# Kernel optimization log

Hardware: AMD Instinct MI355X
Metric: run time of the kernel (lower is better)

Reference implementation:

```python
import jax, jax.numpy as jnp
import numpy as np

B, S, E, D = 8, 2048, 1024, 512

def setup_inputs() -> dict:
    key = jax.random.key(0)
    ks = jax.random.split(key, 7)
    scale = 1.0 / np.sqrt(E)
    return {
        "X": jax.random.normal(ks[0], (B, S, E), dtype=jnp.float32),
        "lam": jnp.float32(0.8),
        "W_q": jax.random.uniform(ks[1], (E, 2 * D), jnp.float32, -scale, scale),
        "b_q": jax.random.uniform(ks[2], (2 * D,), jnp.float32, -scale, scale),
        "W_k": jax.random.uniform(ks[3], (E, 2 * D), jnp.float32, -scale, scale),
        "b_k": jax.random.uniform(ks[4], (2 * D,), jnp.float32, -scale, scale),
        "W_v": jax.random.uniform(ks[5], (E, D), jnp.float32, -scale, scale),
        "b_v": jax.random.uniform(ks[6], (D,), jnp.float32, -scale, scale),
    }

def reference(X, lam, W_q, b_q, W_k, b_k, W_v, b_v):
    # Projections
    Q = X @ W_q + b_q          # [B, S, 2D]
    K = X @ W_k + b_k          # [B, S, 2D]
    V = X @ W_v + b_v          # [B, S, D]
    Q1, Q2 = Q[..., :D], Q[..., D:]
    K1, K2 = K[..., :D], K[..., D:]
    s = 1.0 / np.sqrt(D)
    A1 = jnp.einsum('bqd,bkd->bqk', Q1, K1) * s  # [B, S, S]
    A2 = jnp.einsum('bqd,bkd->bqk', Q2, K2) * s
    P = jax.nn.softmax(A1, axis=-1) - lam * jax.nn.softmax(A2, axis=-1)
    return jnp.einsum('bqk,bkd->bqd', P, V)      # [B, S, D]
```

## Files before the change

kernel.cpp:

```cpp
#include <hip/hip_runtime.h>


typedef unsigned short u16;
typedef short    bf16x8 __attribute__((ext_vector_type(8)));
typedef unsigned short u16x8 __attribute__((ext_vector_type(8)));
typedef unsigned short u16x4 __attribute__((ext_vector_type(4)));
typedef float    f32x4  __attribute__((ext_vector_type(4)));

typedef __attribute__((address_space(3))) unsigned int       lds_uint;
typedef __attribute__((address_space(1))) const unsigned int gl_uint;

__device__ __forceinline__ void glds16(const void* g, void* l) {
  __builtin_amdgcn_global_load_lds((gl_uint*)g, (lds_uint*)l, 16, 0, 0);
}

__device__ __forceinline__ u16 to_bf16(float f) {
  unsigned u = __float_as_uint(f);
  return (u16)((u + 0x7FFFu + ((u >> 16) & 1u)) >> 16);
}
__device__ __forceinline__ float b2f(u16 h) {
  return __uint_as_float(((unsigned)h) << 16);
}


__global__ void cvt_x(const float4* __restrict__ in, u16x4* __restrict__ out, int n4) {
  int i = blockIdx.x * 256 + threadIdx.x;
  if (i >= n4) return;
  float4 v = in[i];
  u16x4 o;
  o[0] = to_bf16(v.x); o[1] = to_bf16(v.y); o[2] = to_bf16(v.z); o[3] = to_bf16(v.w);
  out[i] = o;
}

__global__ void transpose_cvt(const float* __restrict__ in, u16* __restrict__ out,
                              int R, int C) {
  __shared__ float t[64][65];
  int c0 = blockIdx.x * 64, r0 = blockIdx.y * 64;
  int tx = threadIdx.x, ty = threadIdx.y;
  #pragma unroll
  for (int i = 0; i < 64; i += 4)
    t[ty + i][tx] = in[(long)(r0 + ty + i) * C + c0 + tx];
  __syncthreads();
  #pragma unroll
  for (int i = 0; i < 64; i += 4)
    out[(long)(c0 + ty + i) * R + r0 + tx] = to_bf16(t[tx][ty + i]);
}

__global__ void concat2(const float* __restrict__ a, const float* __restrict__ b,
                        float* __restrict__ o, int n) {
  int i = blockIdx.x * 256 + threadIdx.x;
  if (i < n) o[i] = a[i];
  else if (i < 2 * n) o[i] = b[i - n];
}

__device__ __forceinline__ void swizzle_tiles(int& tm, int& tn) {
  int nx = gridDim.x;
  int lin = blockIdx.y * nx + blockIdx.x;
  int span = nx * 4;
  int group = lin / span;
  int ing = lin % span;
  tm = group * 4 + (ing & 3);
  tn = ing >> 2;
}

__global__ __launch_bounds__(256, 4) void gemm_nt(
    const u16* __restrict__ A, int lda,
    const u16* __restrict__ B, int ldb,
    u16* __restrict__ C1, u16* __restrict__ C2, int splitN, int ldc,
    int Kd, float scale,
    const float* __restrict__ bias, int biasMode)
{
  __shared__ u16 SM[2][8192];
  u16* As = SM[0];
  u16* Bs = SM[1];

  int tid = threadIdx.x;
  int wave = tid >> 6, lane = tid & 63;
  int quad = lane >> 4, ln = lane & 15;
  int wm = wave >> 1, wn = wave & 1;
  int tm, tn;
  swizzle_tiles(tm, tn);
  int c8 = lane >> 3, ml = lane & 7;

  const f32x4 fz = {0.f, 0.f, 0.f, 0.f};
  f32x4 acc[4][4];
  #pragma unroll
  for (int i = 0; i < 4; i++)
    #pragma unroll
    for (int j = 0; j < 4; j++) acc[i][j] = fz;

  const u16* Abase = A + (long)(tm * 128 + ml) * lda + c8 * 8;
  const u16* Bbase = B + (long)(tn * 128 + ml) * ldb + c8 * 8;

  for (int kt = 0; kt < Kd; kt += 64) {
    __syncthreads();
    #pragma unroll
    for (int i = 0; i < 4; i++) {
      int mg = wave * 4 + i;
      glds16(Abase + (long)mg * 8 * lda + kt, &As[mg * 512]);
      glds16(Bbase + (long)mg * 8 * ldb + kt, &Bs[mg * 512]);
    }
    __syncthreads();
    #pragma unroll
    for (int ks = 0; ks < 2; ks++) {
      bf16x8 af[4], bfr[4];
      int c = ks * 4 + quad;
      #pragma unroll
      for (int mt = 0; mt < 4; mt++) {
        int m = wm * 64 + mt * 16 + ln;
        af[mt] = *(const bf16x8*)&As[((m >> 3) * 64 + c * 8 + (m & 7)) * 8];
      }
      #pragma unroll
      for (int nt = 0; nt < 4; nt++) {
        int n = wn * 64 + nt * 16 + ln;
        bfr[nt] = *(const bf16x8*)&Bs[((n >> 3) * 64 + c * 8 + (n & 7)) * 8];
      }
      #pragma unroll
      for (int mt = 0; mt < 4; mt++)
        #pragma unroll
        for (int nt = 0; nt < 4; nt++)
          acc[mt][nt] = __builtin_amdgcn_mfma_f32_16x16x32_bf16(af[mt], bfr[nt], acc[mt][nt], 0, 0, 0);
    }
  }

  int rowBase = tm * 128 + wm * 64;
  int colBase = tn * 128 + wn * 64;
  u16* Cw = C1; int outCol = colBase;
  if (colBase >= splitN) { Cw = C2; outCol = colBase - splitN; }
  u16* eb = &SM[0][0] + wave * 4096;

  __syncthreads();
  #pragma unroll
  for (int mt = 0; mt < 4; mt++) {
    #pragma unroll
    for (int nt = 0; nt < 4; nt++) {
      int colL = nt * 16 + ln;
      float bcol = (biasMode == 1) ? bias[colBase + colL] : 0.f;
      #pragma unroll
      for (int r = 0; r < 4; r++) {
        int rowL = mt * 16 + quad * 4 + r;
        float brow = (biasMode == 2) ? bias[rowBase + rowL] : 0.f;
        float v = acc[mt][nt][r] * scale + bcol + brow;
        eb[rowL * 64 + (((colL >> 3) ^ (rowL & 7)) << 3) + (colL & 7)] = to_bf16(v);
      }
    }
  }
  {
    int row = lane;
    long gr = (long)(rowBase + row) * ldc + outCol;
    #pragma unroll
    for (int c = 0; c < 8; c++) {
      u16x8 ch = *(const u16x8*)&eb[row * 64 + ((c ^ (row & 7)) << 3)];
      *(u16x8*)&Cw[gr + c * 8] = ch;
    }
  }
}

__device__ __forceinline__ void gemm256_core(
    const u16* __restrict__ A, int lda,
    const u16* __restrict__ B, int ldb,
    int NT, int tm, int tn, u16* SMp, f32x4 (&acc)[8][4])
{
  int tid = threadIdx.x;
  int wave = tid >> 6, lane = tid & 63;
  int quad = lane >> 4, ln = lane & 15;
  int wm = wave >> 2, wn = wave & 3;
  int c8 = lane >> 3, ml = lane & 7;

  const f32x4 fz = {0.f, 0.f, 0.f, 0.f};
  #pragma unroll
  for (int i = 0; i < 8; i++)
    #pragma unroll
    for (int j = 0; j < 4; j++) acc[i][j] = fz;

  const u16* Ab = A + (long)(tm * 256 + ml) * lda + c8 * 8;
  const u16* Bb = B + (long)(tn * 256 + ml) * ldb + c8 * 8;

  #pragma unroll
  for (int h = 0; h < 2; h++) {
    int hg = h * 16 + wave * 2;
    glds16(Ab + (long)(hg * 8) * lda,       SMp + hg * 512);
    glds16(Ab + (long)(hg * 8 + 8) * lda,   SMp + (hg + 1) * 512);
  }
  #pragma unroll
  for (int h = 0; h < 2; h++) {
    int hg = h * 16 + wave * 2;
    glds16(Bb + (long)(hg * 8) * ldb,       SMp + 32768 + hg * 512);
    glds16(Bb + (long)(hg * 8 + 8) * ldb,   SMp + 32768 + (hg + 1) * 512);
  }
  {
    int kt1 = (NT > 1) ? 64 : 0;
    #pragma unroll
    for (int h = 0; h < 2; h++) {
      int hg = h * 16 + wave * 2;
      glds16(Bb + (long)(hg * 8) * ldb + kt1,     SMp + 49152 + hg * 512);
      glds16(Bb + (long)(hg * 8 + 8) * ldb + kt1, SMp + 49152 + (hg + 1) * 512);
    }
  }
  asm volatile("s_waitcnt vmcnt(4)" ::: "memory");
  __builtin_amdgcn_s_barrier();
  __builtin_amdgcn_sched_barrier(0);

  int bcur = 0;
  for (int t = 0; t < NT; t++) {
    const int p = t & 1;
    const u16* Ar = SMp + p * 16384;
    const u16* Br = SMp + 32768 + bcur * 16384;

    {
      int ktA = ((t + 1 < NT) ? (t + 1) : (NT - 1)) << 6;
      u16* dA = SMp + ((t + 1) & 1) * 16384;
      #pragma unroll
      for (int h = 0; h < 2; h++) {
        int hg = h * 16 + wave * 2;
        glds16(Ab + (long)(hg * 8) * lda + ktA,     dA + hg * 512);
        glds16(Ab + (long)(hg * 8 + 8) * lda + ktA, dA + (hg + 1) * 512);
      }
      int ktB = ((t + 2 < NT) ? (t + 2) : (NT - 1)) << 6;
      int bst = bcur + 2; if (bst >= 3) bst -= 3;
      u16* dB = SMp + 32768 + bst * 16384;
      #pragma unroll
      for (int h = 0; h < 2; h++) {
        int hg = h * 16 + wave * 2;
        glds16(Bb + (long)(hg * 8) * ldb + ktB,     dB + hg * 512);
        glds16(Bb + (long)(hg * 8 + 8) * ldb + ktB, dB + (hg + 1) * 512);
      }
    }
    __builtin_amdgcn_sched_barrier(0);

    bf16x8 bfr[2][4];
    #pragma unroll
    for (int nt = 0; nt < 4; nt++) {
      int n = wn * 64 + nt * 16 + ln;
      #pragma unroll
      for (int ks = 0; ks < 2; ks++)
        bfr[ks][nt] = *(const bf16x8*)(Br + ((n >> 3) * 64 + (ks * 4 + quad) * 8 + (n & 7)) * 8);
    }
    #pragma unroll
    for (int g = 0; g < 4; g++) {
      bf16x8 af[2][2];
      #pragma unroll
      for (int dm = 0; dm < 2; dm++) {
        int m = wm * 128 + (g * 2 + dm) * 16 + ln;
        #pragma unroll
        for (int ks = 0; ks < 2; ks++)
          af[dm][ks] = *(const bf16x8*)(Ar + ((m >> 3) * 64 + (ks * 4 + quad) * 8 + (m & 7)) * 8);
      }
      #pragma unroll
      for (int ks = 0; ks < 2; ks++)
        #pragma unroll
        for (int dm = 0; dm < 2; dm++)
          #pragma unroll
          for (int nt = 0; nt < 4; nt++)
            acc[g * 2 + dm][nt] = __builtin_amdgcn_mfma_f32_16x16x32_bf16(
                af[dm][ks], bfr[ks][nt], acc[g * 2 + dm][nt], 0, 0, 0);
    }

    asm volatile("s_waitcnt vmcnt(4)" ::: "memory");
    __builtin_amdgcn_s_barrier();
    __builtin_amdgcn_sched_barrier(0);
    bcur = (bcur == 2) ? 0 : bcur + 1;
  }
}

__global__ __launch_bounds__(512, 2) void gemm_nt256(
    const u16* __restrict__ A, int lda,
    const u16* __restrict__ B, int ldb,
    u16* __restrict__ C1, u16* __restrict__ C2, int splitN, int ldc,
    int Kd, float scale,
    const float* __restrict__ bias, int biasMode)
{
  __shared__ u16 SM[5][16384];
  int tm, tn;
  swizzle_tiles(tm, tn);
  f32x4 acc[8][4];
  gemm256_core(A, lda, B, ldb, Kd >> 6, tm, tn, &SM[0][0], acc);

  int tid = threadIdx.x;
  int wave = tid >> 6, lane = tid & 63;
  int quad = lane >> 4, ln = lane & 15;
  int wm = wave >> 2, wn = wave & 3;

  int rowBase = tm * 256 + wm * 128;
  int colBase = tn * 256 + wn * 64;
  u16* Cw = C1; int outCol = colBase;
  if (colBase >= splitN) { Cw = C2; outCol = colBase - splitN; }
  u16* eb = &SM[0][0] + wave * 8192;

  asm volatile("s_waitcnt vmcnt(0)" ::: "memory");
  __builtin_amdgcn_s_barrier();
  __builtin_amdgcn_sched_barrier(0);

  #pragma unroll
  for (int mt = 0; mt < 8; mt++) {
    #pragma unroll
    for (int nt = 0; nt < 4; nt++) {
      int colL = nt * 16 + ln;
      float bcol = (biasMode == 1) ? bias[colBase + colL] : 0.f;
      #pragma unroll
      for (int r = 0; r < 4; r++) {
        int rowL = mt * 16 + quad * 4 + r;
        float brow = (biasMode == 2) ? bias[rowBase + rowL] : 0.f;
        float v = acc[mt][nt][r] * scale + bcol + brow;
        eb[rowL * 64 + (((colL >> 3) ^ (rowL & 7)) << 3) + (colL & 7)] = to_bf16(v);
      }
    }
  }
  #pragma unroll
  for (int rr = 0; rr < 2; rr++) {
    int row = rr * 64 + lane;
    long gr = (long)(rowBase + row) * ldc + outCol;
    #pragma unroll
    for (int c = 0; c < 8; c++) {
      u16x8 ch = *(const u16x8*)&eb[row * 64 + ((c ^ (row & 7)) << 3)];
      *(u16x8*)&Cw[gr + c * 8] = ch;
    }
  }
}

__global__ __launch_bounds__(512, 2) void gemm_s256(
    const u16* __restrict__ Q, const u16* __restrict__ K,
    u16* __restrict__ E1, u16* __restrict__ E2,
    float* __restrict__ statsP, float scale)
{
  __shared__ u16 SM[5][16384];
  int bz = blockIdx.z >> 1, half = blockIdx.z & 1;
  const u16* A = Q + (long)bz * 2097152 + half * 512;
  const u16* B = K + (long)bz * 2097152 + half * 512;
  u16* Ed = (half ? E2 : E1) + (long)bz * 4194304;
  statsP += (long)blockIdx.z * 65536;

  int tm, tn;
  swizzle_tiles(tm, tn);
  f32x4 acc[8][4];
  gemm256_core(A, 1024, B, 1024, 8 , tm, tn, &SM[0][0], acc);

  int tid = threadIdx.x;
  int wave = tid >> 6, lane = tid & 63;
  int quad = lane >> 4, ln = lane & 15;
  int wm = wave >> 2, wn = wave & 3;

  int rowBase = tm * 256 + wm * 128;
  int colBase = tn * 256 + wn * 64;
  int kb = tn * 4 + wn;
  u16* eb = &SM[0][0] + wave * 8192;

  asm volatile("s_waitcnt vmcnt(0)" ::: "memory");
  __builtin_amdgcn_s_barrier();
  __builtin_amdgcn_sched_barrier(0);

  #pragma unroll
  for (int mt = 0; mt < 8; mt++) {
    #pragma unroll
    for (int nt = 0; nt < 4; nt++) {
      int colL = nt * 16 + ln;
      #pragma unroll
      for (int r = 0; r < 4; r++) {
        int rowL = mt * 16 + quad * 4 + r;
        eb[rowL * 64 + (((colL >> 3) ^ (rowL & 7)) << 3) + (colL & 7)] =
            to_bf16(__expf(acc[mt][nt][r] * scale));
      }
    }
  }
  #pragma unroll
  for (int rr = 0; rr < 2; rr++) {
    int row = rr * 64 + lane;
    u16x8 ch[8];
    #pragma unroll
    for (int c = 0; c < 8; c++)
      ch[c] = *(const u16x8*)&eb[row * 64 + ((c ^ (row & 7)) << 3)];
    u16* Ep = Ed + (long)(rowBase + row) * 2048 + colBase;
    #pragma unroll
    for (int c = 0; c < 8; c++)
      *(u16x8*)&Ep[c * 8] = ch[c];
    float L = 0.f;
    #pragma unroll
    for (int c = 0; c < 8; c++)
      #pragma unroll
      for (int j = 0; j < 8; j++) L += b2f(ch[c][j]);
    statsP[(rowBase + row) * 32 + kb] = L;
  }
}

__global__ void stats_reduce(const float* __restrict__ sp, float* __restrict__ so,
                             const float* __restrict__ lamPtr) {
  int gid = blockIdx.x * 256 + threadIdx.x;
  const float* p = sp + (long)gid * 32;
  float L = 0.f;
  #pragma unroll
  for (int kb = 0; kb < 32; kb++) L += p[kb];
  int half = (gid >> 11) & 1;
  so[gid] = (half ? lamPtr[0] : 1.0f) / L;
}

__global__ __launch_bounds__(512, 2) void apply_pv(
    const u16* __restrict__ E1, const u16* __restrict__ E2,
    const u16* __restrict__ VT, const float* __restrict__ inv,
    float* __restrict__ Out)
{
  __shared__ u16 Vs[2][32768];
  __shared__ u16 Pb[2][4096];
  __shared__ float i1s[64], i2s[64];

  const int NT = 32;
  int b = blockIdx.x & 7, qt = blockIdx.x >> 3;
  int q0 = qt * 64;
  int tid = threadIdx.x;
  int wave = tid >> 6, lane = tid & 63, quad = lane >> 4, ln = lane & 15;
  int c8 = lane >> 3, ml = lane & 7;
  int r = tid >> 3, cg8 = tid & 7;

  const u16* e1p = E1 + ((long)b * 2048 + q0 + r) * 2048 + cg8 * 8;
  const u16* e2p = E2 + ((long)b * 2048 + q0 + r) * 2048 + cg8 * 8;
  const u16* Vbase = VT + (long)b * 2048;
  int pw = (r >> 3) * 512 + cg8 * 64 + (r & 7) * 8;

  const f32x4 fz = {0.f, 0.f, 0.f, 0.f};
  f32x4 acc[4][4];
  #pragma unroll
  for (int i = 0; i < 4; i++)
    #pragma unroll
    for (int j = 0; j < 4; j++) acc[i][j] = fz;

  if (tid < 64)       i1s[tid]       = inv[(long)(b * 2 + 0) * 2048 + q0 + tid];
  else if (tid < 128) i2s[tid - 64]  = inv[(long)(b * 2 + 1) * 2048 + q0 + (tid - 64)];
  u16x8 a1 = *(const u16x8*)(e1p);
  u16x8 a2 = *(const u16x8*)(e2p);
  __builtin_amdgcn_sched_barrier(0);
  #pragma unroll
  for (int i = 0; i < 8; i++) {
    int dg = wave * 8 + i;
    glds16(Vbase + (long)(dg * 8 + ml) * 16384 + c8 * 8, &Vs[0][dg * 512]);
  }
  __builtin_amdgcn_sched_barrier(0);
  asm volatile("s_waitcnt lgkmcnt(0)" ::: "memory");
  __builtin_amdgcn_s_barrier();
  __builtin_amdgcn_sched_barrier(0);
  float i1 = i1s[r], i2 = i2s[r];
  {
    u16x8 o;
    #pragma unroll
    for (int j = 0; j < 8; j++)
      o[j] = to_bf16(b2f(a1[j]) * i1 - b2f(a2[j]) * i2);
    *(u16x8*)&Pb[0][pw] = o;
  }
  a1 = *(const u16x8*)(e1p + 64);
  a2 = *(const u16x8*)(e2p + 64);
  __builtin_amdgcn_sched_barrier(0);
  asm volatile("s_waitcnt lgkmcnt(0)" ::: "memory");
  asm volatile("s_waitcnt vmcnt(2)" ::: "memory");
  __builtin_amdgcn_sched_barrier(0);
  __builtin_amdgcn_s_barrier();
  __builtin_amdgcn_sched_barrier(0);

  for (int t = 0; t < NT; t++) {
    const int p = t & 1;
    const u16* Vr = &Vs[p][0];
    const u16* Pr = &Pb[p][0];
    u16* Vw = &Vs[p ^ 1][0];
    u16* Pw = &Pb[p ^ 1][0];
    int ktv = ((t + 1 < NT) ? (t + 1) : (NT - 1)) << 6;
    int kte = ((t + 2 < NT) ? (t + 2) : (NT - 1)) << 6;
    bf16x8 vf[2][4];

    #pragma unroll
    for (int q = 0; q < 4; q++) {
      bf16x8 pf[2];
      #pragma unroll
      for (int ks = 0; ks < 2; ks++) {
        int m = q * 16 + ln;
        pf[ks] = *(const bf16x8*)&Pr[((m >> 3) * 64 + (ks * 4 + quad) * 8 + (m & 7)) * 8];
      }
      if (q == 0) {
        #pragma unroll
        for (int ks = 0; ks < 2; ks++)
          #pragma unroll
          for (int nt = 0; nt < 4; nt++) {
            int d = wave * 64 + nt * 16 + ln;
            vf[ks][nt] = *(const bf16x8*)&Vr[((d >> 3) * 64 + (ks * 4 + quad) * 8 + (d & 7)) * 8];
          }
      }
      #pragma unroll
      for (int i = 0; i < 2; i++) {
        int dg = wave * 8 + q * 2 + i;
        glds16(Vbase + (long)(dg * 8 + ml) * 16384 + ktv + c8 * 8, Vw + dg * 512);
      }
      if (q == 3) {
        __builtin_amdgcn_sched_barrier(0);
        u16x8 o;
        #pragma unroll
        for (int j = 0; j < 8; j++)
          o[j] = to_bf16(b2f(a1[j]) * i1 - b2f(a2[j]) * i2);
        *(u16x8*)&Pw[pw] = o;
        a1 = *(const u16x8*)(e1p + kte);
        a2 = *(const u16x8*)(e2p + kte);
      }
      __builtin_amdgcn_sched_barrier(0);
      __builtin_amdgcn_s_barrier();
      asm volatile("s_waitcnt lgkmcnt(0)" ::: "memory");
      __builtin_amdgcn_sched_barrier(0);
      __builtin_amdgcn_s_setprio(1);
      #pragma unroll
      for (int ks = 0; ks < 2; ks++)
        #pragma unroll
        for (int nt = 0; nt < 4; nt++)
          acc[q][nt] = __builtin_amdgcn_mfma_f32_16x16x32_bf16(pf[ks], vf[ks][nt], acc[q][nt], 0, 0, 0);
      __builtin_amdgcn_s_setprio(0);
      __builtin_amdgcn_sched_barrier(0);
      if (q == 3) asm volatile("s_waitcnt vmcnt(2)" ::: "memory");
      __builtin_amdgcn_s_barrier();
      __builtin_amdgcn_sched_barrier(0);
    }
  }

  #pragma unroll
  for (int mt = 0; mt < 4; mt++)
    #pragma unroll
    for (int nt = 0; nt < 4; nt++)
      #pragma unroll
      for (int r2 = 0; r2 < 4; r2++)
        Out[((long)b * 2048 + q0 + mt * 16 + quad * 4 + r2) * 512 + wave * 64 + nt * 16 + ln] =
            acc[mt][nt][r2];
}


extern "C" void kernel_launch(void* const* d_in, const int* in_sizes, int n_in,
                              void* d_out, int out_size, void* d_ws, size_t ws_size,
                              hipStream_t stream)
{
  const float* X   = (const float*)d_in[0];
  const float* lam = (const float*)d_in[1];
  const float* Wq  = (const float*)d_in[2];
  const float* bq  = (const float*)d_in[3];
  const float* Wk  = (const float*)d_in[4];
  const float* bk  = (const float*)d_in[5];
  const float* Wv  = (const float*)d_in[6];
  const float* bv  = (const float*)d_in[7];
  float* Out = (float*)d_out;
  char* ws = (char*)d_ws;

  u16*  WqkT   = (u16*)(ws + 0);
  u16*  WvT    = (u16*)(ws + 4194304);
  float* bqk   = (float*)(ws + 5242880);
  u16*  Qb     = (u16*)(ws + 6291456);
  u16*  Kb     = (u16*)(ws + 39845888);
  u16*  VTb    = (u16*)(ws + 73400320);
  u16*  Xb     = (u16*)(ws + 90177536);
  u16*  E1     = (u16*)(ws + 90177536);
  u16*  E2     = (u16*)(ws + 157286400);
  float* statsP= (float*)(ws + 224395264);
  float* invD  = (float*)(ws + 228589568);

  cvt_x<<<16384, 256, 0, stream>>>((const float4*)X, (u16x4*)Xb, 4194304);
  transpose_cvt<<<dim3(16, 16), dim3(64, 4), 0, stream>>>(Wq, WqkT, 1024, 1024);
  transpose_cvt<<<dim3(16, 16), dim3(64, 4), 0, stream>>>(Wk, WqkT + 1024 * 1024, 1024, 1024);
  transpose_cvt<<<dim3(8, 16),  dim3(64, 4), 0, stream>>>(Wv, WvT, 1024, 512);
  concat2<<<8, 256, 0, stream>>>(bq, bk, bqk, 1024);

  gemm_nt256<<<dim3(8, 64), 512, 0, stream>>>(Xb, 1024, WqkT, 1024,
                                              Qb, Kb, 1024, 1024,
                                              1024, 1.0f, bqk, 1);
  gemm_nt<<<dim3(128, 4), 256, 0, stream>>>(WvT, 1024, Xb, 1024,
                                            VTb, VTb, 1 << 30, 16384,
                                            1024, 1.0f, bv, 2);

  const float s = 0.044194173824159216f;
  gemm_s256<<<dim3(8, 8, 16), 512, 0, stream>>>(Qb, Kb, E1, E2, statsP, s);

  stats_reduce<<<128, 256, 0, stream>>>(statsP, invD, lam);
  apply_pv<<<256, 512, 0, stream>>>(E1, E2, VTb, invD, Out);
}
```

Before: 478.9 us.

## Make 256-tile GEMMs persistent over multiple M tiles with continuous prefetch pipeline

Both the QK projection GEMM and the scores GEMM now have each block walk several consecutive 256-row M tiles against one B column tile, using a single flattened K-loop with K-step 32. Prefetch continues across tile boundaries, so the pipeline does not drain and refill between tiles, and the epilogue runs inline every 16 or 32 steps using a dedicated LDS staging region. Grids shrink from 512/1024 blocks to 256 blocks, and the old tile swizzle is dropped. In exchange, each K-step does half as many MFMAs per barrier, there are fewer blocks to hide latency, and the inline epilogue stalls the prefetch pipeline while it runs.

```diff
diff --git a/kernel.cpp b/kernel.cpp
--- a/kernel.cpp
+++ b/kernel.cpp
@@ -156,230 +156,250 @@
   }
 }
 
-__device__ __forceinline__ void gemm256_core(
-    const u16* __restrict__ A, int lda,
-    const u16* __restrict__ B, int ldb,
-    int NT, int tm, int tn, u16* SMp, f32x4 (&acc)[8][4])
-{
-  int tid = threadIdx.x;
-  int wave = tid >> 6, lane = tid & 63;
-  int quad = lane >> 4, ln = lane & 15;
-  int wm = wave >> 2, wn = wave & 3;
-  int c8 = lane >> 3, ml = lane & 7;
-
-  const f32x4 fz = {0.f, 0.f, 0.f, 0.f};
-  #pragma unroll
-  for (int i = 0; i < 8; i++)
-    #pragma unroll
-    for (int j = 0; j < 4; j++) acc[i][j] = fz;
-
-  const u16* Ab = A + (long)(tm * 256 + ml) * lda + c8 * 8;
-  const u16* Bb = B + (long)(tn * 256 + ml) * ldb + c8 * 8;
-
-  #pragma unroll
-  for (int h = 0; h < 2; h++) {
-    int hg = h * 16 + wave * 2;
-    glds16(Ab + (long)(hg * 8) * lda,       SMp + hg * 512);
-    glds16(Ab + (long)(hg * 8 + 8) * lda,   SMp + (hg + 1) * 512);
-  }
-  #pragma unroll
-  for (int h = 0; h < 2; h++) {
-    int hg = h * 16 + wave * 2;
-    glds16(Bb + (long)(hg * 8) * ldb,       SMp + 32768 + hg * 512);
-    glds16(Bb + (long)(hg * 8 + 8) * ldb,   SMp + 32768 + (hg + 1) * 512);
-  }
-  {
-    int kt1 = (NT > 1) ? 64 : 0;
-    #pragma unroll
-    for (int h = 0; h < 2; h++) {
-      int hg = h * 16 + wave * 2;
-      glds16(Bb + (long)(hg * 8) * ldb + kt1,     SMp + 49152 + hg * 512);
-      glds16(Bb + (long)(hg * 8 + 8) * ldb + kt1, SMp + 49152 + (hg + 1) * 512);
-    }
-  }
-  asm volatile("s_waitcnt vmcnt(4)" ::: "memory");
-  __builtin_amdgcn_s_barrier();
-  __builtin_amdgcn_sched_barrier(0);
-
-  int bcur = 0;
-  for (int t = 0; t < NT; t++) {
-    const int p = t & 1;
-    const u16* Ar = SMp + p * 16384;
-    const u16* Br = SMp + 32768 + bcur * 16384;
-
-    {
-      int ktA = ((t + 1 < NT) ? (t + 1) : (NT - 1)) << 6;
-      u16* dA = SMp + ((t + 1) & 1) * 16384;
-      #pragma unroll
-      for (int h = 0; h < 2; h++) {
-        int hg = h * 16 + wave * 2;
-        glds16(Ab + (long)(hg * 8) * lda + ktA,     dA + hg * 512);
-        glds16(Ab + (long)(hg * 8 + 8) * lda + ktA, dA + (hg + 1) * 512);
-      }
-      int ktB = ((t + 2 < NT) ? (t + 2) : (NT - 1)) << 6;
-      int bst = bcur + 2; if (bst >= 3) bst -= 3;
-      u16* dB = SMp + 32768 + bst * 16384;
-      #pragma unroll
-      for (int h = 0; h < 2; h++) {
-        int hg = h * 16 + wave * 2;
-        glds16(Bb + (long)(hg * 8) * ldb + ktB,     dB + hg * 512);
-        glds16(Bb + (long)(hg * 8 + 8) * ldb + ktB, dB + (hg + 1) * 512);
-      }
-    }
-    __builtin_amdgcn_sched_barrier(0);
-
-    bf16x8 bfr[2][4];
-    #pragma unroll
-    for (int nt = 0; nt < 4; nt++) {
-      int n = wn * 64 + nt * 16 + ln;
-      #pragma unroll
-      for (int ks = 0; ks < 2; ks++)
-        bfr[ks][nt] = *(const bf16x8*)(Br + ((n >> 3) * 64 + (ks * 4 + quad) * 8 + (n & 7)) * 8);
-    }
-    #pragma unroll
-    for (int g = 0; g < 4; g++) {
-      bf16x8 af[2][2];
-      #pragma unroll
-      for (int dm = 0; dm < 2; dm++) {
-        int m = wm * 128 + (g * 2 + dm) * 16 + ln;
-        #pragma unroll
-        for (int ks = 0; ks < 2; ks++)
-          af[dm][ks] = *(const bf16x8*)(Ar + ((m >> 3) * 64 + (ks * 4 + quad) * 8 + (m & 7)) * 8);
-      }
-      #pragma unroll
-      for (int ks = 0; ks < 2; ks++)
-        #pragma unroll
-        for (int dm = 0; dm < 2; dm++)
-          #pragma unroll
-          for (int nt = 0; nt < 4; nt++)
-            acc[g * 2 + dm][nt] = __builtin_amdgcn_mfma_f32_16x16x32_bf16(
-                af[dm][ks], bfr[ks][nt], acc[g * 2 + dm][nt], 0, 0, 0);
-    }
-
-    asm volatile("s_waitcnt vmcnt(4)" ::: "memory");
-    __builtin_amdgcn_s_barrier();
-    __builtin_amdgcn_sched_barrier(0);
-    bcur = (bcur == 2) ? 0 : bcur + 1;
-  }
-}
-
-__global__ __launch_bounds__(512, 2) void gemm_nt256(
-    const u16* __restrict__ A, int lda,
-    const u16* __restrict__ B, int ldb,
-    u16* __restrict__ C1, u16* __restrict__ C2, int splitN, int ldc,
-    int Kd, float scale,
-    const float* __restrict__ bias, int biasMode)
-{
-  __shared__ u16 SM[5][16384];
-  int tm, tn;
-  swizzle_tiles(tm, tn);
-  f32x4 acc[8][4];
-  gemm256_core(A, lda, B, ldb, Kd >> 6, tm, tn, &SM[0][0], acc);
-
-  int tid = threadIdx.x;
-  int wave = tid >> 6, lane = tid & 63;
-  int quad = lane >> 4, ln = lane & 15;
-  int wm = wave >> 2, wn = wave & 3;
-
-  int rowBase = tm * 256 + wm * 128;
-  int colBase = tn * 256 + wn * 64;
-  u16* Cw = C1; int outCol = colBase;
-  if (colBase >= splitN) { Cw = C2; outCol = colBase - splitN; }
-  u16* eb = &SM[0][0] + wave * 8192;
-
-  asm volatile("s_waitcnt vmcnt(0)" ::: "memory");
-  __builtin_amdgcn_s_barrier();
-  __builtin_amdgcn_sched_barrier(0);
-
-  #pragma unroll
-  for (int mt = 0; mt < 8; mt++) {
-    #pragma unroll
-    for (int nt = 0; nt < 4; nt++) {
-      int colL = nt * 16 + ln;
-      float bcol = (biasMode == 1) ? bias[colBase + colL] : 0.f;
-      #pragma unroll
-      for (int r = 0; r < 4; r++) {
-        int rowL = mt * 16 + quad * 4 + r;
-        float brow = (biasMode == 2) ? bias[rowBase + rowL] : 0.f;
-        float v = acc[mt][nt][r] * scale + bcol + brow;
-        eb[rowL * 64 + (((colL >> 3) ^ (rowL & 7)) << 3) + (colL & 7)] = to_bf16(v);
-      }
-    }
-  }
-  #pragma unroll
-  for (int rr = 0; rr < 2; rr++) {
-    int row = rr * 64 + lane;
-    long gr = (long)(rowBase + row) * ldc + outCol;
-    #pragma unroll
-    for (int c = 0; c < 8; c++) {
-      u16x8 ch = *(const u16x8*)&eb[row * 64 + ((c ^ (row & 7)) << 3)];
-      *(u16x8*)&Cw[gr + c * 8] = ch;
-    }
-  }
-}
-
-__global__ __launch_bounds__(512, 2) void gemm_s256(
+
+__global__ __launch_bounds__(512, 2) void gemm_s256p(
     const u16* __restrict__ Q, const u16* __restrict__ K,
     u16* __restrict__ E1, u16* __restrict__ E2,
     float* __restrict__ statsP, float scale)
 {
-  __shared__ u16 SM[5][16384];
+  __shared__ u16 SM[73728];
+
   int bz = blockIdx.z >> 1, half = blockIdx.z & 1;
   const u16* A = Q + (long)bz * 2097152 + half * 512;
   const u16* B = K + (long)bz * 2097152 + half * 512;
   u16* Ed = (half ? E2 : E1) + (long)bz * 4194304;
-  statsP += (long)blockIdx.z * 65536;
-
-  int tm, tn;
-  swizzle_tiles(tm, tn);
+  float* sp = statsP + (long)blockIdx.z * 65536;
+
+  int tn = blockIdx.x;
+  int tmg = blockIdx.y;
+  int tid = threadIdx.x;
+  int wave = tid >> 6, lane = tid & 63, quad = lane >> 4, ln = lane & 15;
+  int wm = wave >> 2, wn = wave & 3;
+  int dr = ((lane >> 5) << 3) + (lane & 7);
+  int cg = (lane >> 3) & 3;
+
+  const f32x4 fz = {0.f, 0.f, 0.f, 0.f};
   f32x4 acc[8][4];
-  gemm256_core(A, 1024, B, 1024, 8 , tm, tn, &SM[0][0], acc);
-
+  #pragma unroll
+  for (int i = 0; i < 8; i++)
+    #pragma unroll
+    for (int j = 0; j < 4; j++) acc[i][j] = fz;
+
+  const u16* Abase = A + (long)(tmg * 1024 + wave * 32 + dr) * 1024 + cg * 8;
+  const u16* Bbase = B + (long)(tn * 256 + wave * 32 + dr) * 1024 + cg * 8;
+  u16* ldsA0 = SM;
+  u16* ldsB0 = SM + 16384;
+  u16* eb = SM + 40960 + wave * 4096;
+
+  glds16(Abase,                ldsA0 + wave * 1024);
+  glds16(Abase + 16 * 1024,    ldsA0 + wave * 1024 + 512);
+  glds16(Bbase,                ldsB0 + wave * 1024);
+  glds16(Bbase + 16 * 1024,    ldsB0 + wave * 1024 + 512);
+  glds16(Bbase + 32,           ldsB0 + 8192 + wave * 1024);
+  glds16(Bbase + 16 * 1024 + 32, ldsB0 + 8192 + wave * 1024 + 512);
+  asm volatile("s_waitcnt vmcnt(2)" ::: "memory");
+  __builtin_amdgcn_s_barrier();
+  __builtin_amdgcn_sched_barrier(0);
+
+  for (int T = 0; T < 64; T++) {
+    const u16* Ar = ldsA0 + (T & 1) * 8192;
+    const u16* Br = ldsB0 + (T % 3) * 8192;
+
+    {
+      int Ta = (T + 1 < 64) ? T + 1 : 63;
+      long roff = (long)((Ta >> 4) * 256) * 1024 + ((Ta & 15) << 5);
+      u16* dA = ldsA0 + (Ta & 1) * 8192 + wave * 1024;
+      glds16(Abase + roff,             dA);
+      glds16(Abase + roff + 16 * 1024, dA + 512);
+      int Tb = (T + 2 < 64) ? T + 2 : 63;
+      int ktB = (Tb & 15) << 5;
+      u16* dB = ldsB0 + (Tb % 3) * 8192 + wave * 1024;
+      glds16(Bbase + ktB,             dB);
+      glds16(Bbase + ktB + 16 * 1024, dB + 512);
+    }
+    __builtin_amdgcn_sched_barrier(0);
+
+    bf16x8 bfr[4];
+    #pragma unroll
+    for (int nt = 0; nt < 4; nt++) {
+      int n = wn * 64 + nt * 16 + ln;
+      bfr[nt] = *(const bf16x8*)(Br + ((n >> 3) * 32 + quad * 8 + (n & 7)) * 8);
+    }
+    #pragma unroll
+    for (int g = 0; g < 8; g++) {
+      int m = wm * 128 + g * 16 + ln;
+      bf16x8 af = *(const bf16x8*)(Ar + ((m >> 3) * 32 + quad * 8 + (m & 7)) * 8);
+      #pragma unroll
+      for (int nt = 0; nt < 4; nt++)
+        acc[g][nt] = __builtin_amdgcn_mfma_f32_16x16x32_bf16(af, bfr[nt], acc[g][nt], 0, 0, 0);
+    }
+
+    asm volatile("s_waitcnt vmcnt(2)" ::: "memory");
+    __builtin_amdgcn_s_barrier();
+    __builtin_amdgcn_sched_barrier(0);
+
+    if ((T & 15) == 15) {
+      int sub = T >> 4;
+      int rowBaseW = (tmg * 4 + sub) * 256 + wm * 128;
+      int colBase = tn * 256 + wn * 64;
+      int kb = tn * 4 + wn;
+      #pragma unroll
+      for (int h = 0; h < 2; h++) {
+        #pragma unroll
+        for (int mt = 0; mt < 4; mt++) {
+          #pragma unroll
+          for (int nt = 0; nt < 4; nt++) {
+            int colL = nt * 16 + ln;
+            #pragma unroll
+            for (int r = 0; r < 4; r++) {
+              int rowL = mt * 16 + quad * 4 + r;
+              eb[rowL * 64 + (((colL >> 3) ^ (rowL & 7)) << 3) + (colL & 7)] =
+                  to_bf16(__expf(acc[h * 4 + mt][nt][r] * scale));
+            }
+          }
+        }
+        {
+          int row = lane;
+          u16x8 ch[8];
+          #pragma unroll
+          for (int c = 0; c < 8; c++)
+            ch[c] = *(const u16x8*)&eb[row * 64 + ((c ^ (row & 7)) << 3)];
+          u16* Ep = Ed + (long)(rowBaseW + h * 64 + row) * 2048 + colBase;
+          #pragma unroll
+          for (int c = 0; c < 8; c++)
+            *(u16x8*)&Ep[c * 8] = ch[c];
+          float L = 0.f;
+          #pragma unroll
+          for (int c = 0; c < 8; c++)
+            #pragma unroll
+            for (int j = 0; j < 8; j++) L += b2f(ch[c][j]);
+          sp[(rowBaseW + h * 64 + row) * 32 + kb] = L;
+        }
+      }
+      #pragma unroll
+      for (int i = 0; i < 8; i++)
+        #pragma unroll
+        for (int j = 0; j < 4; j++) acc[i][j] = fz;
+    }
+  }
+  asm volatile("s_waitcnt vmcnt(0)" ::: "memory");
+}
+
+__global__ __launch_bounds__(512, 2) void gemm_nt256p(
+    const u16* __restrict__ A, const u16* __restrict__ B,
+    u16* __restrict__ C1, u16* __restrict__ C2, int splitN, int ldc,
+    float scale, const float* __restrict__ bias, int biasMode)
+{
+  __shared__ u16 SM[73728];
+
+  int tn = blockIdx.x;
+  int tmg = blockIdx.y;
   int tid = threadIdx.x;
-  int wave = tid >> 6, lane = tid & 63;
-  int quad = lane >> 4, ln = lane & 15;
+  int wave = tid >> 6, lane = tid & 63, quad = lane >> 4, ln = lane & 15;
   int wm = wave >> 2, wn = wave & 3;
-
-  int rowBase = tm * 256 + wm * 128;
-  int colBase = tn * 256 + wn * 64;
-  int kb = tn * 4 + wn;
-  u16* eb = &SM[0][0] + wave * 8192;
-
+  int dr = ((lane >> 5) << 3) + (lane & 7);
+  int cg = (lane >> 3) & 3;
+
+  const f32x4 fz = {0.f, 0.f, 0.f, 0.f};
+  f32x4 acc[8][4];
+  #pragma unroll
+  for (int i = 0; i < 8; i++)
+    #pragma unroll
+    for (int j = 0; j < 4; j++) acc[i][j] = fz;
+
+  const u16* Abase = A + (long)(tmg * 512 + wave * 32 + dr) * 1024 + cg * 8;
+  const u16* Bbase = B + (long)(tn * 256 + wave * 32 + dr) * 1024 + cg * 8;
+  u16* ldsA0 = SM;
+  u16* ldsB0 = SM + 16384;
+  u16* eb = SM + 40960 + wave * 4096;
+
+  glds16(Abase,                  ldsA0 + wave * 1024);
+  glds16(Abase + 16 * 1024,      ldsA0 + wave * 1024 + 512);
+  glds16(Bbase,                  ldsB0 + wave * 1024);
+  glds16(Bbase + 16 * 1024,      ldsB0 + wave * 1024 + 512);
+  glds16(Bbase + 32,             ldsB0 + 8192 + wave * 1024);
+  glds16(Bbase + 16 * 1024 + 32, ldsB0 + 8192 + wave * 1024 + 512);
+  asm volatile("s_waitcnt vmcnt(2)" ::: "memory");
+  __builtin_amdgcn_s_barrier();
+  __builtin_amdgcn_sched_barrier(0);
+
+  for (int T = 0; T < 64; T++) {
+    const u16* Ar = ldsA0 + (T & 1) * 8192;
+    const u16* Br = ldsB0 + (T % 3) * 8192;
+
+    {
+      int Ta = (T + 1 < 64) ? T + 1 : 63;
+      long roff = (long)((Ta >> 5) * 256) * 1024 + ((Ta & 31) << 5);
+      u16* dA = ldsA0 + (Ta & 1) * 8192 + wave * 1024;
+      glds16(Abase + roff,             dA);
+      glds16(Abase + roff + 16 * 1024, dA + 512);
+      int Tb = (T + 2 < 64) ? T + 2 : 63;
+      int ktB = (Tb & 31) << 5;
+      u16* dB = ldsB0 + (Tb % 3) * 8192 + wave * 1024;
+      glds16(Bbase + ktB,             dB);
+      glds16(Bbase + ktB + 16 * 1024, dB + 512);
+    }
+    __builtin_amdgcn_sched_barrier(0);
+
+    bf16x8 bfr[4];
+    #pragma unroll
+    for (int nt = 0; nt < 4; nt++) {
+      int n = wn * 64 + nt * 16 + ln;
+      bfr[nt] = *(const bf16x8*)(Br + ((n >> 3) * 32 + quad * 8 + (n & 7)) * 8);
+    }
+    #pragma unroll
+    for (int g = 0; g < 8; g++) {
+      int m = wm * 128 + g * 16 + ln;
+      bf16x8 af = *(const bf16x8*)(Ar + ((m >> 3) * 32 + quad * 8 + (m & 7)) * 8);
+      #pragma unroll
+      for (int nt = 0; nt < 4; nt++)
+        acc[g][nt] = __builtin_amdgcn_mfma_f32_16x16x32_bf16(af, bfr[nt], acc[g][nt], 0, 0, 0);
+    }
+
+    asm volatile("s_waitcnt vmcnt(2)" ::: "memory");
+    __builtin_amdgcn_s_barrier();
+    __builtin_amdgcn_sched_barrier(0);
+
+    if ((T & 31) == 31) {
+      int sub = T >> 5;
+      int rowBaseW = (tmg * 2 + sub) * 256 + wm * 128;
+      int colBase = tn * 256 + wn * 64;
+      u16* Cw = C1; int outCol = colBase;
+      if (colBase >= splitN) { Cw = C2; outCol = colBase - splitN; }
+      #pragma unroll
+      for (int h = 0; h < 2; h++) {
+        #pragma unroll
+        for (int mt = 0; mt < 4; mt++) {
+          #pragma unroll
+          for (int nt = 0; nt < 4; nt++) {
+            int colL = nt * 16 + ln;
+            float bcol = (biasMode == 1) ? bias[colBase + colL] : 0.f;
+            #pragma unroll
+            for (int r = 0; r < 4; r++) {
+              int rowL = mt * 16 + quad * 4 + r;
+              float brow = (biasMode == 2) ? bias[rowBaseW + h * 64 + rowL] : 0.f;
+              float v = acc[h * 4 + mt][nt][r] * scale + bcol + brow;
+              eb[rowL * 64 + (((colL >> 3) ^ (rowL & 7)) << 3) + (colL & 7)] = to_bf16(v);
+            }
+          }
+        }
+        {
+          int row = lane;
+          long gr = (long)(rowBaseW + h * 64 + row) * ldc + outCol;
+          #pragma unroll
+          for (int c = 0; c < 8; c++) {
+            u16x8 ch = *(const u16x8*)&eb[row * 64 + ((c ^ (row & 7)) << 3)];
+            *(u16x8*)&Cw[gr + c * 8] = ch;
+          }
+        }
+      }
+      #pragma unroll
+      for (int i = 0; i < 8; i++)
+        #pragma unroll
+        for (int j = 0; j < 4; j++) acc[i][j] = fz;
+    }
+  }
   asm volatile("s_waitcnt vmcnt(0)" ::: "memory");
-  __builtin_amdgcn_s_barrier();
-  __builtin_amdgcn_sched_barrier(0);
-
-  #pragma unroll
-  for (int mt = 0; mt < 8; mt++) {
-    #pragma unroll
-    for (int nt = 0; nt < 4; nt++) {
-      int colL = nt * 16 + ln;
-      #pragma unroll
-      for (int r = 0; r < 4; r++) {
-        int rowL = mt * 16 + quad * 4 + r;
-        eb[rowL * 64 + (((colL >> 3) ^ (rowL & 7)) << 3) + (colL & 7)] =
-            to_bf16(__expf(acc[mt][nt][r] * scale));
-      }
-    }
-  }
-  #pragma unroll
-  for (int rr = 0; rr < 2; rr++) {
-    int row = rr * 64 + lane;
-    u16x8 ch[8];
-    #pragma unroll
-    for (int c = 0; c < 8; c++)
-      ch[c] = *(const u16x8*)&eb[row * 64 + ((c ^ (row & 7)) << 3)];
-    u16* Ep = Ed + (long)(rowBase + row) * 2048 + colBase;
-    #pragma unroll
-    for (int c = 0; c < 8; c++)
-      *(u16x8*)&Ep[c * 8] = ch[c];
-    float L = 0.f;
-    #pragma unroll
-    for (int c = 0; c < 8; c++)
-      #pragma unroll
-      for (int j = 0; j < 8; j++) L += b2f(ch[c][j]);
-    statsP[(rowBase + row) * 32 + kb] = L;
-  }
 }
 
 __global__ void stats_reduce(const float* __restrict__ sp, float* __restrict__ so,
@@ -557,15 +577,14 @@
   transpose_cvt<<<dim3(8, 16),  dim3(64, 4), 0, stream>>>(Wv, WvT, 1024, 512);
   concat2<<<8, 256, 0, stream>>>(bq, bk, bqk, 1024);
 
-  gemm_nt256<<<dim3(8, 64), 512, 0, stream>>>(Xb, 1024, WqkT, 1024,
-                                              Qb, Kb, 1024, 1024,
-                                              1024, 1.0f, bqk, 1);
+  gemm_nt256p<<<dim3(8, 32), 512, 0, stream>>>(Xb, WqkT, Qb, Kb, 1024, 1024,
+                                               1.0f, bqk, 1);
   gemm_nt<<<dim3(128, 4), 256, 0, stream>>>(WvT, 1024, Xb, 1024,
                                             VTb, VTb, 1 << 30, 16384,
                                             1024, 1.0f, bv, 2);
 
   const float s = 0.044194173824159216f;
-  gemm_s256<<<dim3(8, 8, 16), 512, 0, stream>>>(Qb, Kb, E1, E2, statsP, s);
+  gemm_s256p<<<dim3(8, 2, 16), 512, 0, stream>>>(Qb, Kb, E1, E2, statsP, s);
 
   stats_reduce<<<128, 256, 0, stream>>>(statsP, invD, lam);
   apply_pv<<<256, 512, 0, stream>>>(E1, E2, VTb, invD, Out);
```

Result: no change. 474.9 us (-0.8%).
